# Kernel tuning notes

Hardware: AMD Instinct MI355X
Metric: run time of the kernel (lower is better)

The kernel has to match this reference:

```python
import jax, jax.numpy as jnp
import numpy as np

T_OUT = 12  # num_timesteps_output


def setup_inputs() -> dict:
    key = jax.random.key(0)
    ks = jax.random.split(key, 12)
    B, N, T, F = 32, 325, 12, 2
    C, H = 10, 64
    s = 0.08  # weight init scale (~1/sqrt(H)) to keep gates in sane range
    return {
        "A": jnp.zeros((N, N), jnp.float32),
        "X": jax.random.normal(ks[0], (B, N, T, F), jnp.float32),
        "enc_Wih": jax.random.normal(ks[1], (C, 3 * H, F), jnp.float32) * s,
        "enc_Whh": jax.random.normal(ks[2], (C, 3 * H, H), jnp.float32) * s,
        "enc_bih": jax.random.normal(ks[3], (C, 3 * H), jnp.float32) * s,
        "enc_bhh": jax.random.normal(ks[4], (C, 3 * H), jnp.float32) * s,
        "dec_Wih": jax.random.normal(ks[5], (C, 3 * H, 1), jnp.float32) * s,
        "dec_Whh": jax.random.normal(ks[6], (C, 3 * H, H), jnp.float32) * s,
        "dec_bih": jax.random.normal(ks[7], (C, 3 * H), jnp.float32) * s,
        "dec_bhh": jax.random.normal(ks[8], (C, 3 * H), jnp.float32) * s,
        "lin_W": jax.random.normal(ks[9], (C, 1, H), jnp.float32) * s,
        "lin_b": jax.random.normal(ks[10], (C, 1), jnp.float32) * s,
        "embed": jax.random.normal(ks[11], (N, C), jnp.float32),
    }


def _gru_update(gi, gh, h, H):
    # PyTorch GRU gate order: r, z, n
    r = jax.nn.sigmoid(gi[..., :H] + gh[..., :H])
    z = jax.nn.sigmoid(gi[..., H:2 * H] + gh[..., H:2 * H])
    n = jnp.tanh(gi[..., 2 * H:] + r * gh[..., 2 * H:])
    return (1.0 - z) * n + z * h


def reference(A, X, enc_Wih, enc_Whh, enc_bih, enc_bhh,
              dec_Wih, dec_Whh, dec_bih, dec_bhh, lin_W, lin_b, embed):
    B, N, T, F = X.shape
    C = enc_Wih.shape[0]
    H = enc_Whh.shape[-1]
    BN = B * N

    # (T, BN, F): time-major, batch*nodes flattened (matches X.view(-1,T,F).permute(1,0,2))
    Xs = jnp.transpose(X.reshape(BN, T, F), (1, 0, 2))

    def enc_step(h, x_t):  # h: (C, BN, H), x_t: (BN, F)
        gi = jnp.einsum('bf,cgf->cbg', x_t, enc_Wih) + enc_bih[:, None, :]
        gh = jnp.einsum('cbh,cgh->cbg', h, enc_Whh) + enc_bhh[:, None, :]
        return _gru_update(gi, gh, h, H), None

    h0 = jnp.zeros((C, BN, H), X.dtype)
    h_enc, _ = jax.lax.scan(enc_step, h0, Xs)  # (C, BN, H)

    # initial decoder input: last observed value of feature 0
    lv0 = jnp.broadcast_to(Xs[-1, :, 0][None, :, None], (C, BN, 1))

    def dec_step(carry, _):
        h, lv = carry
        gi = jnp.einsum('cbf,cgf->cbg', lv, dec_Wih) + dec_bih[:, None, :]
        gh = jnp.einsum('cbh,cgh->cbg', h, dec_Whh) + dec_bhh[:, None, :]
        h = _gru_update(gi, gh, h, H)
        value = jnp.einsum('cbh,coh->cbo', h, lin_W) + lin_b[:, None, :]  # (C, BN, 1)
        # original does last_value = value.detach()
        return (h, jax.lax.stop_gradient(value)), value

    (_, _), vals = jax.lax.scan(dec_step, (h_enc, lv0), None, length=T_OUT)
    # vals: (T_out, C, BN, 1) -> (B, N, T_out, C)
    out = jnp.transpose(vals[..., 0], (2, 0, 1)).reshape(B, N, T_OUT, C)

    weight = jax.nn.softmax(embed, axis=-1)  # (N, C)
    return jnp.einsum('bntc,nc->bnt', out, weight)
```

## Files before the change

### kernel.cpp

```cpp
#include <hip/hip_runtime.h>
#include <math.h>

#define N_   325
#define BN_  10400
#define R_   32

typedef _Float16 h8v __attribute__((ext_vector_type(8)));
typedef float    f4v __attribute__((ext_vector_type(4)));

#define L1C  1.4426950408889634f
#define L2C  2.8853900817779268f

__device__ __forceinline__ float rcp_f(float x){ return __builtin_amdgcn_rcpf(x); }
#if __has_builtin(__builtin_amdgcn_exp2f)
__device__ __forceinline__ float exp2_f(float x){ return __builtin_amdgcn_exp2f(x); }
#else
__device__ __forceinline__ float exp2_f(float x){ return __expf(x * 0.6931471805599453f); }
#endif

__device__ __forceinline__ int plane_idx(int m,int k){
    return m*64 + ((((k>>3)^(m&7))<<3)|(k&7));
}
__device__ __forceinline__ int frag_idx(int m,int kb){
    return m*64 + ((kb^(m&7))<<3);
}

__device__ __forceinline__ void load_B_scaled(const float* __restrict__ Whh,
                                              int jcol, int kg, h8v Bf[3][2])
{
    const float sc[3] = { -L1C, -L1C, -L2C };
#pragma unroll
    for (int g3=0; g3<3; ++g3)
#pragma unroll
        for (int ch=0; ch<2; ++ch) {
            const float* p = Whh + (g3*64 + jcol)*64 + ch*32 + kg*8;
            float4 a = *(const float4*)p;
            float4 b = *(const float4*)(p+4);
            h8v v;
            v[0]=(_Float16)(sc[g3]*a.x); v[1]=(_Float16)(sc[g3]*a.y);
            v[2]=(_Float16)(sc[g3]*a.z); v[3]=(_Float16)(sc[g3]*a.w);
            v[4]=(_Float16)(sc[g3]*b.x); v[5]=(_Float16)(sc[g3]*b.y);
            v[6]=(_Float16)(sc[g3]*b.z); v[7]=(_Float16)(sc[g3]*b.w);
            Bf[g3][ch] = v;
        }
}

__global__ void __launch_bounds__(256, 4) krnn_kernel(
    const float* __restrict__ X,
    const float* __restrict__ eWih, const float* __restrict__ eWhh,
    const float* __restrict__ ebih, const float* __restrict__ ebhh,
    const float* __restrict__ dWih, const float* __restrict__ dWhh,
    const float* __restrict__ dbih, const float* __restrict__ dbhh,
    const float* __restrict__ linW, const float* __restrict__ linb,
    const float* __restrict__ embed, float* __restrict__ out)
{
    __shared__ _Float16 sH[2][R_*64];
    __shared__ float2 sX2[12*R_];
    __shared__ float sWgt[R_];

    const int c    = blockIdx.y;
    const int row0 = blockIdx.x * R_;
    const int tid  = threadIdx.x;
    const int lane = tid & 63;
    const int wv   = tid >> 6;
    const int nl   = lane & 15;
    const int kg   = lane >> 4;
    const int jcol = wv*16 + nl;

    for (int i = tid; i < 12*R_; i += 256) {
        int t = i >> 5, m = i & (R_-1);
        const float* p = X + (size_t)(row0+m)*24 + 2*t;
        sX2[i] = make_float2(p[0], p[1]);
    }
    for (int i = tid; i < R_*64; i += 256) sH[1][i] = (_Float16)0.0f;
    if (tid < R_) {
        int n = (row0 + tid) % N_;
        float e[10], mx = -1e30f;
#pragma unroll
        for (int cc=0; cc<10; ++cc){ e[cc]=embed[n*10+cc]; mx=fmaxf(mx,e[cc]); }
        float den = 0.0f;
#pragma unroll
        for (int cc=0; cc<10; ++cc) den += exp2_f((e[cc]-mx)*L1C);
        sWgt[tid] = exp2_f((e[c]-mx)*L1C) * rcp_f(den);
    }

    h8v Bf[3][2];
    load_B_scaled(eWhh + c*12288, jcol, kg, Bf);

    h8v BeR, BeZ, BeN, BeN2;
#pragma unroll
    for (int i=0;i<8;++i){ BeR[i]=(_Float16)0.0f; BeZ[i]=(_Float16)0.0f;
                           BeN[i]=(_Float16)0.0f; BeN2[i]=(_Float16)0.0f; }
    if (kg == 0) {
        int gc = jcol;
        BeR[0]=(_Float16)(-L1C*eWih[c*384 + gc*2]);
        BeR[1]=(_Float16)(-L1C*eWih[c*384 + gc*2 + 1]);
        BeR[2]=(_Float16)(-L1C*(ebih[c*192+gc] + ebhh[c*192+gc]));
        gc = 64 + jcol;
        BeZ[0]=(_Float16)(-L1C*eWih[c*384 + gc*2]);
        BeZ[1]=(_Float16)(-L1C*eWih[c*384 + gc*2 + 1]);
        BeZ[2]=(_Float16)(-L1C*(ebih[c*192+gc] + ebhh[c*192+gc]));
        gc = 128 + jcol;
        BeN[0]=(_Float16)(-L2C*eWih[c*384 + gc*2]);
        BeN[1]=(_Float16)(-L2C*eWih[c*384 + gc*2 + 1]);
        BeN[2]=(_Float16)(-L2C*ebih[c*192+gc]);
        BeN2[2]=(_Float16)(-L2C*ebhh[c*192+gc]);
    }
    h8v Ae[2];
#pragma unroll
    for (int Mt=0;Mt<2;++Mt){
#pragma unroll
        for (int i=0;i<8;++i) Ae[Mt][i]=(_Float16)0.0f;
        if (kg==0) Ae[Mt][2]=(_Float16)1.0f;
    }

    const f4v Z0 = {0.0f,0.0f,0.0f,0.0f};

    float hreg[2][4];
#pragma unroll
    for (int Mt=0;Mt<2;++Mt)
#pragma unroll
        for (int r4=0;r4<4;++r4) hreg[Mt][r4]=0.0f;

    __syncthreads();

    for (int t = 0; t < 12; ++t) {
        const int rp = (t+1)&1, wp = t&1;
        h8v Ah[2][2];
#pragma unroll
        for (int Mt=0; Mt<2; ++Mt)
#pragma unroll
            for (int ch=0; ch<2; ++ch)
                Ah[Mt][ch] = *(const h8v*)&sH[rp][frag_idx(Mt*16+nl, ch*4+kg)];

        if (kg == 0) {
#pragma unroll
            for (int Mt=0; Mt<2; ++Mt) {
                float2 xe = sX2[t*R_ + Mt*16 + nl];
                Ae[Mt][0] = (_Float16)xe.x; Ae[Mt][1] = (_Float16)xe.y;
            }
        }

        f4v a0[2], a1[2], a2[2], a3[2];
#pragma unroll
        for (int Mt=0;Mt<2;++Mt) {
            a0[Mt] = __builtin_amdgcn_mfma_f32_16x16x32_f16(Ae[Mt], BeR,  Z0, 0,0,0);
            a1[Mt] = __builtin_amdgcn_mfma_f32_16x16x32_f16(Ae[Mt], BeZ,  Z0, 0,0,0);
            a2[Mt] = __builtin_amdgcn_mfma_f32_16x16x32_f16(Ae[Mt], BeN2, Z0, 0,0,0);
            a3[Mt] = __builtin_amdgcn_mfma_f32_16x16x32_f16(Ae[Mt], BeN,  Z0, 0,0,0);
#pragma unroll
            for (int ch=0; ch<2; ++ch) {
                a0[Mt] = __builtin_amdgcn_mfma_f32_16x16x32_f16(Ah[Mt][ch], Bf[0][ch], a0[Mt],0,0,0);
                a1[Mt] = __builtin_amdgcn_mfma_f32_16x16x32_f16(Ah[Mt][ch], Bf[1][ch], a1[Mt],0,0,0);
                a2[Mt] = __builtin_amdgcn_mfma_f32_16x16x32_f16(Ah[Mt][ch], Bf[2][ch], a2[Mt],0,0,0);
            }
        }

#pragma unroll
        for (int Mt=0;Mt<2;++Mt)
#pragma unroll
            for (int r4=0;r4<4;++r4) {
                int m = Mt*16 + kg*4 + r4;
                float r  = rcp_f(1.0f + exp2_f(a0[Mt][r4]));
                float z  = rcp_f(1.0f + exp2_f(a1[Mt][r4]));
                float e  = exp2_f(fmaf(r, a2[Mt][r4], a3[Mt][r4]));
                float nn = fmaf(2.0f, rcp_f(1.0f + e), -1.0f);
                float hnew = nn + z*(hreg[Mt][r4] - nn);
                hreg[Mt][r4] = hnew;
                sH[wp][plane_idx(m,jcol)] = (_Float16)hnew;
            }
        __syncthreads();
    }

    load_B_scaled(dWhh + c*12288, jcol, kg, Bf);
    h8v Blw[2];
#pragma unroll
    for (int ch=0; ch<2; ++ch) {
        const float* p = linW + c*64 + ch*32 + kg*8;
        float4 a = *(const float4*)p;
        float4 b = *(const float4*)(p+4);
        h8v v;
        v[0]=(_Float16)a.x; v[1]=(_Float16)a.y; v[2]=(_Float16)a.z; v[3]=(_Float16)a.w;
        v[4]=(_Float16)b.x; v[5]=(_Float16)b.y; v[6]=(_Float16)b.z; v[7]=(_Float16)b.w;
        Blw[ch] = v;
    }
    float dws0, ks0, dws1, ks1, dwn2, kn, cbh2;
    {
        int gc = jcol;
        dws0 = -L1C*dWih[c*192 + gc];
        ks0  = -L1C*(dbih[c*192 + gc] + dbhh[c*192 + gc]);
        gc = 64 + jcol;
        dws1 = -L1C*dWih[c*192 + gc];
        ks1  = -L1C*(dbih[c*192 + gc] + dbhh[c*192 + gc]);
        gc = 128 + jcol;
        dwn2 = -L2C*dWih[c*192 + gc];
        kn   = -L2C*dbih[c*192 + gc];
        cbh2 = -L2C*dbhh[c*192 + gc];
    }
    const float lb = linb[c];

    float lvx[2][4];
#pragma unroll
    for (int Mt=0;Mt<2;++Mt)
#pragma unroll
        for (int r4=0;r4<4;++r4)
            lvx[Mt][r4] = sX2[11*R_ + Mt*16 + kg*4 + r4].x;

    for (int s = 0; s < 12; ++s) {
        const int rp = (s+1)&1, wp = s&1;
        h8v Ah[2][2];
#pragma unroll
        for (int Mt=0; Mt<2; ++Mt)
#pragma unroll
            for (int ch=0; ch<2; ++ch)
                Ah[Mt][ch] = *(const h8v*)&sH[rp][frag_idx(Mt*16+nl, ch*4+kg)];

        f4v a0[2], a1[2], a2[2], av[2];
#pragma unroll
        for (int Mt=0;Mt<2;++Mt) {
            a0[Mt] = __builtin_amdgcn_mfma_f32_16x16x32_f16(Ah[Mt][0], Bf[0][0], Z0, 0,0,0);
            a1[Mt] = __builtin_amdgcn_mfma_f32_16x16x32_f16(Ah[Mt][0], Bf[1][0], Z0, 0,0,0);
            a2[Mt] = __builtin_amdgcn_mfma_f32_16x16x32_f16(Ah[Mt][0], Bf[2][0], Z0, 0,0,0);
            a0[Mt] = __builtin_amdgcn_mfma_f32_16x16x32_f16(Ah[Mt][1], Bf[0][1], a0[Mt],0,0,0);
            a1[Mt] = __builtin_amdgcn_mfma_f32_16x16x32_f16(Ah[Mt][1], Bf[1][1], a1[Mt],0,0,0);
            a2[Mt] = __builtin_amdgcn_mfma_f32_16x16x32_f16(Ah[Mt][1], Bf[2][1], a2[Mt],0,0,0);
        }
        if (s > 0) {
#pragma unroll
            for (int Mt=0;Mt<2;++Mt) {
                av[Mt] = __builtin_amdgcn_mfma_f32_16x16x32_f16(Ah[Mt][0], Blw[0], Z0, 0,0,0);
                av[Mt] = __builtin_amdgcn_mfma_f32_16x16x32_f16(Ah[Mt][1], Blw[1], av[Mt],0,0,0);
            }
        }

#pragma unroll
        for (int Mt=0;Mt<2;++Mt)
#pragma unroll
            for (int r4=0;r4<4;++r4) {
                int m = Mt*16 + kg*4 + r4;
                float lv;
                if (s == 0) lv = lvx[Mt][r4];
                else {
                    lv = av[Mt][r4] + lb;
                    if (wv == 0 && nl == 0)
                        atomicAdd(&out[(size_t)(row0+m)*12 + (s-1)], sWgt[m]*lv);
                }
                float r  = rcp_f(1.0f + exp2_f(a0[Mt][r4] + fmaf(dws0, lv, ks0)));
                float z  = rcp_f(1.0f + exp2_f(a1[Mt][r4] + fmaf(dws1, lv, ks1)));
                float e  = exp2_f(fmaf(r, a2[Mt][r4] + cbh2, fmaf(dwn2, lv, kn)));
                float nn = fmaf(2.0f, rcp_f(1.0f + e), -1.0f);
                float hnew = nn + z*(hreg[Mt][r4] - nn);
                hreg[Mt][r4] = hnew;
                sH[wp][plane_idx(m,jcol)] = (_Float16)hnew;
            }
        __syncthreads();
    }

    {
        f4v av[2];
#pragma unroll
        for (int Mt=0; Mt<2; ++Mt) {
            h8v A0 = *(const h8v*)&sH[1][frag_idx(Mt*16+nl, 0*4+kg)];
            h8v A1 = *(const h8v*)&sH[1][frag_idx(Mt*16+nl, 1*4+kg)];
            av[Mt] = __builtin_amdgcn_mfma_f32_16x16x32_f16(A0, Blw[0], Z0, 0,0,0);
            av[Mt] = __builtin_amdgcn_mfma_f32_16x16x32_f16(A1, Blw[1], av[Mt],0,0,0);
        }
        if (wv == 0 && nl == 0) {
#pragma unroll
            for (int Mt=0;Mt<2;++Mt)
#pragma unroll
                for (int r4=0;r4<4;++r4) {
                    int m = Mt*16 + kg*4 + r4;
                    float v = av[Mt][r4] + lb;
                    atomicAdd(&out[(size_t)(row0+m)*12 + 11], sWgt[m]*v);
                }
        }
    }
}

extern "C" void kernel_launch(void* const* d_in, const int* in_sizes, int n_in,
                              void* d_out, int out_size, void* d_ws, size_t ws_size,
                              hipStream_t stream) {
    const float* X    = (const float*)d_in[1];
    const float* eWih = (const float*)d_in[2];
    const float* eWhh = (const float*)d_in[3];
    const float* ebih = (const float*)d_in[4];
    const float* ebhh = (const float*)d_in[5];
    const float* dWih = (const float*)d_in[6];
    const float* dWhh = (const float*)d_in[7];
    const float* dbih = (const float*)d_in[8];
    const float* dbhh = (const float*)d_in[9];
    const float* linW = (const float*)d_in[10];
    const float* linb = (const float*)d_in[11];
    const float* emb  = (const float*)d_in[12];
    float* out = (float*)d_out;

    hipMemsetAsync(d_out, 0, (size_t)out_size * sizeof(float), stream);

    dim3 grid(BN_ / R_, 10);
    krnn_kernel<<<grid, dim3(256), 0, stream>>>(
        X, eWih, eWhh, ebih, ebhh, dWih, dWhh, dbih, dbhh, linW, linb, emb, out);
}
```

Measured before the change: 233.0 us.

## Fuse GRU gate reciprocals and replace output atomics with workspace reduction

The GRU update is rewritten so the z-gate sigmoid and the tanh share a single reciprocal, computing h_new as a combined numerator over (1+e_n)(1+e_z). This cuts transcendental/rcp instructions per element. The per-cluster atomicAdd accumulation into the output is replaced with plain stores into a per-cluster workspace slice, followed by a second small kernel that sums the 10 slices. That also removes the memset. The trade is an extra kernel launch and more global memory traffic, and the new algebraic form may behave differently under overflow when exp terms are large.

```diff
diff --git a/kernel.cpp b/kernel.cpp
--- a/kernel.cpp
+++ b/kernel.cpp
@@ -4,6 +4,7 @@
 #define N_   325
 #define BN_  10400
 #define R_   32
+#define OUTSZ_ (BN_*12)
 
 typedef _Float16 h8v __attribute__((ext_vector_type(8)));
 typedef float    f4v __attribute__((ext_vector_type(4)));
@@ -52,7 +53,7 @@
     const float* __restrict__ dWih, const float* __restrict__ dWhh,
     const float* __restrict__ dbih, const float* __restrict__ dbhh,
     const float* __restrict__ linW, const float* __restrict__ linb,
-    const float* __restrict__ embed, float* __restrict__ out)
+    const float* __restrict__ embed, float* __restrict__ ws)
 {
     __shared__ _Float16 sH[2][R_*64];
     __shared__ float2 sX2[12*R_];
@@ -161,11 +162,16 @@
 #pragma unroll
             for (int r4=0;r4<4;++r4) {
                 int m = Mt*16 + kg*4 + r4;
-                float r  = rcp_f(1.0f + exp2_f(a0[Mt][r4]));
-                float z  = rcp_f(1.0f + exp2_f(a1[Mt][r4]));
-                float e  = exp2_f(fmaf(r, a2[Mt][r4], a3[Mt][r4]));
-                float nn = fmaf(2.0f, rcp_f(1.0f + e), -1.0f);
-                float hnew = nn + z*(hreg[Mt][r4] - nn);
+                float er = exp2_f(a0[Mt][r4]);
+                float rr = rcp_f(1.0f + er);
+                float ez = exp2_f(a1[Mt][r4]);
+                float en = exp2_f(fmaf(rr, a2[Mt][r4], a3[Mt][r4]));
+                float h  = hreg[Mt][r4];
+                float aa = 1.0f + ez;
+                float den = fmaf(en, aa, aa);
+                float t1 = fmaf(-en, ez, ez);
+                float t2 = fmaf(en, h, h);
+                float hnew = (t1 + t2) * rcp_f(den);
                 hreg[Mt][r4] = hnew;
                 sH[wp][plane_idx(m,jcol)] = (_Float16)hnew;
             }
@@ -198,6 +204,7 @@
         cbh2 = -L2C*dbhh[c*192 + gc];
     }
     const float lb = linb[c];
+    float* __restrict__ wsc = ws + (size_t)c * OUTSZ_;
 
     float lvx[2][4];
 #pragma unroll
@@ -243,13 +250,18 @@
                 else {
                     lv = av[Mt][r4] + lb;
                     if (wv == 0 && nl == 0)
-                        atomicAdd(&out[(size_t)(row0+m)*12 + (s-1)], sWgt[m]*lv);
+                        wsc[(size_t)(row0+m)*12 + (s-1)] = sWgt[m]*lv;
                 }
-                float r  = rcp_f(1.0f + exp2_f(a0[Mt][r4] + fmaf(dws0, lv, ks0)));
-                float z  = rcp_f(1.0f + exp2_f(a1[Mt][r4] + fmaf(dws1, lv, ks1)));
-                float e  = exp2_f(fmaf(r, a2[Mt][r4] + cbh2, fmaf(dwn2, lv, kn)));
-                float nn = fmaf(2.0f, rcp_f(1.0f + e), -1.0f);
-                float hnew = nn + z*(hreg[Mt][r4] - nn);
+                float er = exp2_f(a0[Mt][r4] + fmaf(dws0, lv, ks0));
+                float rr = rcp_f(1.0f + er);
+                float ez = exp2_f(a1[Mt][r4] + fmaf(dws1, lv, ks1));
+                float en = exp2_f(fmaf(rr, a2[Mt][r4] + cbh2, fmaf(dwn2, lv, kn)));
+                float h  = hreg[Mt][r4];
+                float aa = 1.0f + ez;
+                float den = fmaf(en, aa, aa);
+                float t1 = fmaf(-en, ez, ez);
+                float t2 = fmaf(en, h, h);
+                float hnew = (t1 + t2) * rcp_f(den);
                 hreg[Mt][r4] = hnew;
                 sH[wp][plane_idx(m,jcol)] = (_Float16)hnew;
             }
@@ -271,10 +283,21 @@
 #pragma unroll
                 for (int r4=0;r4<4;++r4) {
                     int m = Mt*16 + kg*4 + r4;
-                    float v = av[Mt][r4] + lb;
-                    atomicAdd(&out[(size_t)(row0+m)*12 + 11], sWgt[m]*v);
+                    wsc[(size_t)(row0+m)*12 + 11] = sWgt[m]*(av[Mt][r4] + lb);
                 }
         }
+    }
+}
+
+__global__ void __launch_bounds__(256) mix_kernel(const float* __restrict__ ws,
+                                                  float* __restrict__ out)
+{
+    int i = blockIdx.x * 256 + threadIdx.x;
+    if (i < OUTSZ_) {
+        float s = 0.0f;
+#pragma unroll
+        for (int c = 0; c < 10; ++c) s += ws[(size_t)c * OUTSZ_ + i];
+        out[i] = s;
     }
 }
 
@@ -293,11 +316,11 @@
     const float* linW = (const float*)d_in[10];
     const float* linb = (const float*)d_in[11];
     const float* emb  = (const float*)d_in[12];
+    float* ws  = (float*)d_ws;
     float* out = (float*)d_out;
-
-    hipMemsetAsync(d_out, 0, (size_t)out_size * sizeof(float), stream);
 
     dim3 grid(BN_ / R_, 10);
     krnn_kernel<<<grid, dim3(256), 0, stream>>>(
-        X, eWih, eWhh, ebih, ebhh, dWih, dWhh, dbih, dbhh, linW, linb, emb, out);
-}
+        X, eWih, eWhh, ebih, ebhh, dWih, dWhh, dbih, dbhh, linW, linb, emb, ws);
+    mix_kernel<<<(OUTSZ_ + 255) / 256, dim3(256), 0, stream>>>(ws, out);
+}
```

New measurement: 227.1 us, median of 2. -2.5%, faster.
